# Performance work log

Measured on AMD Instinct MI355X. Metric: run time of the kernel, lower is better.

Reference implementation:

```python
import jax, jax.numpy as jnp
import numpy as np

D, N_EXP, TOP_K = 2048, 64, 8
B, S = 4, 4096

def setup_inputs() -> dict:
    key = jax.random.key(0)
    k1, k2, k3, k4 = jax.random.split(key, 4)
    hidden_states = jax.random.normal(k1, (B, S, D), dtype=jnp.float32)
    # nn.Linear weights are [out, in]; default init ~ U(-1/sqrt(d), 1/sqrt(d))
    bound = 1.0 / np.sqrt(D)
    W_gate = jax.random.uniform(k2, (N_EXP, D), jnp.float32, -bound, bound)
    W_noise = 0.01 * jax.random.normal(k3, (N_EXP, D), dtype=jnp.float32)
    # training-mode noise (router_step % top_k == 0 path): fixed-seed randn
    noise = jax.random.normal(k4, (B, S, N_EXP), dtype=jnp.float32)
    return {"hidden_states": hidden_states, "W_gate": W_gate,
            "W_noise": W_noise, "noise": noise}

def reference(hidden_states, W_gate, W_noise, noise):
    # logits = h @ W_gate^T  : [B,S,n_exp]
    logits = jnp.einsum('bsd,ed->bse', hidden_states, W_gate)
    scale = jax.nn.softplus(jnp.einsum('bsd,ed->bse', hidden_states, W_noise))
    logits = logits + noise * scale
    gates = jax.nn.softmax(logits, axis=-1)
    vals, inds = jax.lax.top_k(gates, TOP_K)  # sorted desc (torch used sorted=False)
    return vals, inds, gates
```

## Files before the change

kernel.cpp:

```cpp
#include <hip/hip_runtime.h>
#include <math.h>

typedef __attribute__((ext_vector_type(8))) _Float16 half8;
typedef __attribute__((ext_vector_type(4))) float    f32x4;

constexpr int D_DIM = 2048;
constexpr int NEXP  = 64;
constexpr int TOPK  = 8;
constexpr int NTOK  = 16384;
constexpr int TM    = 32;
constexpr int BK    = 64;
constexpr int NCH   = D_DIM / BK;
constexpr int OSTR  = 132;
constexpr int NSTR  = 68;
constexpr float WSCALE  = 4096.0f;
constexpr float INV_WSC = 1.0f / 4096.0f;

__device__ __forceinline__ unsigned short f16b(float x) {
    _Float16 h = (_Float16)x;
    return __builtin_bit_cast(unsigned short, h);
}
__device__ __forceinline__ float f16tof(unsigned short b) {
    return (float)__builtin_bit_cast(_Float16, b);
}

__global__ void prep_w(const float* __restrict__ Wg, const float* __restrict__ Wn,
                       unsigned short* __restrict__ wsB)
{
    const int idx = blockIdx.x * blockDim.x + threadIdx.x;
    const int n   = idx >> 8;
    const int K8  = idx & 255;
    const float* src = (n < 64) ? (Wg + (size_t)n * D_DIM)
                                : (Wn + (size_t)(n - 64) * D_DIM);
    float4 a = *reinterpret_cast<const float4*>(src + K8 * 8);
    float4 b = *reinterpret_cast<const float4*>(src + K8 * 8 + 4);

    float v[8] = {a.x, a.y, a.z, a.w, b.x, b.y, b.z, b.w};
    union { unsigned short u[8]; half8 s; } H, L;
#pragma unroll
    for (int j = 0; j < 8; ++j) {
        float xs = v[j] * WSCALE;
        unsigned short h = f16b(xs);
        H.u[j] = h;
        L.u[j] = f16b(xs - f16tof(h));
    }
    const int l = ((K8 & 3) * 16) + (n & 15);
    const size_t base = (size_t)(K8 >> 2) * 8192 + (size_t)(n >> 4) * 1024 + (size_t)l * 8;
    *reinterpret_cast<half8*>(wsB + base)       = H.s;
    *reinterpret_cast<half8*>(wsB + base + 512) = L.s;
}

__global__ __launch_bounds__(512, 4)
void noisy_topk_router(const float* __restrict__ hs,
                       const unsigned short* __restrict__ wsB,
                       const float* __restrict__ nz,
                       float* __restrict__ out)
{
    __shared__ __align__(16) char smem[16896 + 8704];
    unsigned short* stage  = reinterpret_cast<unsigned short*>(smem);
    float*          logits = reinterpret_cast<float*>(smem);
    float*          ldsN   = reinterpret_cast<float*>(smem + 16896);

    const int tid  = threadIdx.x;
    const int lane = tid & 63;
    const int w    = tid >> 6;
    const int t0   = blockIdx.x * TM;

    const int r  = tid >> 4;
    const int k4 = (tid & 15) * 4;
    const float* hrow = hs + (size_t)(t0 + r) * D_DIM + k4;
    const int ks_s = k4 >> 5;
    const int kk   = k4 & 31;
    const int j0   = kk >> 3;
    const int pos  = kk & 7;
    const int mt_s = r >> 4;
    const int m_s  = r & 15;
    const int wroff = (mt_s * 2 + ks_s) * 512 + (j0 * 16 + m_s) * 8 + pos;

    f32x4 accH0[2], accH1[2], accX[2];
#pragma unroll
    for (int mt = 0; mt < 2; ++mt) {
        accH0[mt] = (f32x4){0.f, 0.f, 0.f, 0.f};
        accH1[mt] = (f32x4){0.f, 0.f, 0.f, 0.f};
        accX[mt]  = (f32x4){0.f, 0.f, 0.f, 0.f};
    }

    auto cvt_write = [&](float4 v, unsigned short* buf) {
        float p[4] = {v.x, v.y, v.z, v.w};
        unsigned int Hp[2], Lp[2];
#pragma unroll
        for (int q = 0; q < 2; ++q) {
            unsigned short h0 = f16b(p[2*q]);
            unsigned short h1 = f16b(p[2*q+1]);
            unsigned short l0 = f16b(p[2*q]   - f16tof(h0));
            unsigned short l1 = f16b(p[2*q+1] - f16tof(h1));
            Hp[q] = (unsigned int)h0 | ((unsigned int)h1 << 16);
            Lp[q] = (unsigned int)l0 | ((unsigned int)l1 << 16);
        }
        *reinterpret_cast<uint2*>(buf + wroff)        = make_uint2(Hp[0], Hp[1]);
        *reinterpret_cast<uint2*>(buf + 2048 + wroff) = make_uint2(Lp[0], Lp[1]);
    };

    cvt_write(*reinterpret_cast<const float4*>(hrow), stage);
    __syncthreads();

    for (int c = 0; c < NCH; ++c) {
        float4 pf;
        if (c + 1 < NCH)
            pf = *reinterpret_cast<const float4*>(hrow + (c + 1) * BK);

        const unsigned short* sb = stage + (c & 1) * 4096;

#pragma unroll
        for (int ks = 0; ks < 2; ++ks) {
            const unsigned short* bp = wsB + (size_t)(2 * c + ks) * 8192
                                           + (size_t)w * 1024 + (size_t)lane * 8;
            half8 bhi = *reinterpret_cast<const half8*>(bp);
            half8 blo = *reinterpret_cast<const half8*>(bp + 512);
#pragma unroll
            for (int mt = 0; mt < 2; ++mt) {
                half8 ahi = *reinterpret_cast<const half8*>(sb + (mt * 2 + ks) * 512 + lane * 8);
                half8 alo = *reinterpret_cast<const half8*>(sb + 2048 + (mt * 2 + ks) * 512 + lane * 8);
                if (ks == 0)
                    accH0[mt] = __builtin_amdgcn_mfma_f32_16x16x32_f16(ahi, bhi, accH0[mt], 0, 0, 0);
                else
                    accH1[mt] = __builtin_amdgcn_mfma_f32_16x16x32_f16(ahi, bhi, accH1[mt], 0, 0, 0);
                accX[mt] = __builtin_amdgcn_mfma_f32_16x16x32_f16(ahi, blo, accX[mt], 0, 0, 0);
                accX[mt] = __builtin_amdgcn_mfma_f32_16x16x32_f16(alo, bhi, accX[mt], 0, 0, 0);
            }
        }

        if (c + 1 < NCH)
            cvt_write(pf, stage + ((c + 1) & 1) * 4096);
        __syncthreads();
    }

    {
        const int colb = w * 16 + (lane & 15);
        const int rowb = (lane >> 4) * 4;
#pragma unroll
        for (int mt = 0; mt < 2; ++mt)
#pragma unroll
            for (int rr = 0; rr < 4; ++rr)
                logits[(mt * 16 + rowb + rr) * OSTR + colb] =
                    (accH0[mt][rr] + accH1[mt][rr] + accX[mt][rr]) * INV_WSC;
    }
    {
        const int rr = tid >> 4;
        const int cc = tid & 15;
        float4 v = *reinterpret_cast<const float4*>(nz + (size_t)(t0 + rr) * NEXP + cc * 4);
        *reinterpret_cast<float4*>(&ldsN[rr * NSTR + cc * 4]) = v;
    }
    __syncthreads();

    if (tid < TM) {
        const int tok = t0 + tid;
        float l[NEXP];
        float mx = -3.0e38f;
#pragma unroll
        for (int e = 0; e < NEXP; ++e) {
            float gsc = logits[tid * OSTR + e];
            float nl  = logits[tid * OSTR + 64 + e];
            float sp  = fmaxf(nl, 0.0f) + log1pf(expf(-fabsf(nl)));
            float le  = fmaf(ldsN[tid * NSTR + e], sp, gsc);
            l[e] = le;
            mx = fmaxf(mx, le);
        }
        float sum = 0.0f;
#pragma unroll
        for (int e = 0; e < NEXP; ++e) { float p = expf(l[e] - mx); l[e] = p; sum += p; }
        float inv = 1.0f / sum;
#pragma unroll
        for (int e = 0; e < NEXP; ++e) l[e] *= inv;

#pragma unroll
        for (int e = 0; e < NEXP; ++e) logits[tid * OSTR + e] = l[e];

        float* vout = out + (size_t)tok * TOPK;
        float* iout = out + (size_t)NTOK * TOPK + (size_t)tok * TOPK;
#pragma unroll
        for (int p = 0; p < TOPK; ++p) {
            float m = -1.0f; int mi = 0;
#pragma unroll
            for (int e = 0; e < NEXP; ++e) {
                bool gt = l[e] > m;
                m  = gt ? l[e] : m;
                mi = gt ? e : mi;
            }
            vout[p] = m;
            iout[p] = (float)mi;
#pragma unroll
            for (int e = 0; e < NEXP; ++e) l[e] = (e == mi) ? -1.0f : l[e];
        }
    }
    __syncthreads();

    {
        const int rr = tid >> 4;
        const int cc = tid & 15;
        float* gout = out + (size_t)NTOK * TOPK * 2;
        float4 v = *reinterpret_cast<const float4*>(&logits[rr * OSTR + cc * 4]);
        *reinterpret_cast<float4*>(&gout[(size_t)(t0 + rr) * NEXP + cc * 4]) = v;
    }
}

extern "C" void kernel_launch(void* const* d_in, const int* in_sizes, int n_in,
                              void* d_out, int out_size, void* d_ws, size_t ws_size,
                              hipStream_t stream) {
    const float* hs = (const float*)d_in[0];
    const float* Wg = (const float*)d_in[1];
    const float* Wn = (const float*)d_in[2];
    const float* nz = (const float*)d_in[3];
    float* out = (float*)d_out;
    unsigned short* wsB = (unsigned short*)d_ws;

    prep_w<<<64, 512, 0, stream>>>(Wg, Wn, wsB);
    noisy_topk_router<<<NTOK / TM, 512, 0, stream>>>(hs, wsB, nz, out);
}
```

Baseline: 245.0 us.

## Retile router GEMM with register-prefetched weights and wave-parallel softmax/top-k epilogue

Doubles the K chunk to 128 and re-partitions waves so each wave covers one M tile and two N tiles, reusing each A fragment across two B tiles. Weight fragments are held in registers and prefetched two k-steps ahead, and the LDS staging layout gets an XOR swizzle to reduce bank conflicts. The epilogue now spreads softmax and top-k over all waves using lane-per-expert shuffle reductions, where before only 32 threads did serial per-token loops. The cost is more live registers and twice the LDS staging space, which could lower occupancy under the 512x4 launch bounds.

```diff
diff --git a/kernel.cpp b/kernel.cpp
--- a/kernel.cpp
+++ b/kernel.cpp
@@ -9,10 +9,10 @@
 constexpr int TOPK  = 8;
 constexpr int NTOK  = 16384;
 constexpr int TM    = 32;
-constexpr int BK    = 64;
+constexpr int BK    = 128;
 constexpr int NCH   = D_DIM / BK;
+constexpr int NKS   = D_DIM / 32;
 constexpr int OSTR  = 132;
-constexpr int NSTR  = 68;
 constexpr float WSCALE  = 4096.0f;
 constexpr float INV_WSC = 1.0f / 4096.0f;
 
@@ -56,151 +56,167 @@
                        const float* __restrict__ nz,
                        float* __restrict__ out)
 {
-    __shared__ __align__(16) char smem[16896 + 8704];
+    __shared__ __align__(16) char smem[32768];
     unsigned short* stage  = reinterpret_cast<unsigned short*>(smem);
     float*          logits = reinterpret_cast<float*>(smem);
-    float*          ldsN   = reinterpret_cast<float*>(smem + 16896);
 
     const int tid  = threadIdx.x;
     const int lane = tid & 63;
     const int w    = tid >> 6;
+    const int mt   = w & 1;
+    const int np   = w >> 1;
     const int t0   = blockIdx.x * TM;
 
-    const int r  = tid >> 4;
-    const int k4 = (tid & 15) * 4;
-    const float* hrow = hs + (size_t)(t0 + r) * D_DIM + k4;
-    const int ks_s = k4 >> 5;
-    const int kk   = k4 & 31;
-    const int j0   = kk >> 3;
-    const int pos  = kk & 7;
-    const int mt_s = r >> 4;
-    const int m_s  = r & 15;
-    const int wroff = (mt_s * 2 + ks_s) * 512 + (j0 * 16 + m_s) * 8 + pos;
-
-    f32x4 accH0[2], accH1[2], accX[2];
-#pragma unroll
-    for (int mt = 0; mt < 2; ++mt) {
-        accH0[mt] = (f32x4){0.f, 0.f, 0.f, 0.f};
-        accH1[mt] = (f32x4){0.f, 0.f, 0.f, 0.f};
-        accX[mt]  = (f32x4){0.f, 0.f, 0.f, 0.f};
-    }
-
-    auto cvt_write = [&](float4 v, unsigned short* buf) {
-        float p[4] = {v.x, v.y, v.z, v.w};
-        unsigned int Hp[2], Lp[2];
-#pragma unroll
-        for (int q = 0; q < 2; ++q) {
-            unsigned short h0 = f16b(p[2*q]);
-            unsigned short h1 = f16b(p[2*q+1]);
-            unsigned short l0 = f16b(p[2*q]   - f16tof(h0));
-            unsigned short l1 = f16b(p[2*q+1] - f16tof(h1));
-            Hp[q] = (unsigned int)h0 | ((unsigned int)h1 << 16);
-            Lp[q] = (unsigned int)l0 | ((unsigned int)l1 << 16);
-        }
-        *reinterpret_cast<uint2*>(buf + wroff)        = make_uint2(Hp[0], Hp[1]);
-        *reinterpret_cast<uint2*>(buf + 2048 + wroff) = make_uint2(Lp[0], Lp[1]);
+    const int j0r = lane >> 4;
+    const int mr  = lane & 15;
+    const int j4  = (j0r & 1) << 2;
+
+    const int r    = tid >> 4;
+    const int q    = tid & 15;
+    const int ks_s = q >> 2;
+    const int j0s  = q & 3;
+    const int ms   = r & 15;
+    const int mts  = r >> 4;
+    const int fs   = ks_s | ((j0s & 1) << 2);
+    const int wroff = (mts * 4 + ks_s) * 512 + (j0s * 16 + (ms ^ fs)) * 8;
+    const float* hrow = hs + (size_t)(t0 + r) * D_DIM + q * 8;
+
+    const unsigned short* bbase = wsB + (size_t)np * 2048 + (size_t)lane * 8;
+
+    f32x4 accP0[2], accP1[2], accX0[2], accX1[2];
+#pragma unroll
+    for (int nt = 0; nt < 2; ++nt) {
+        accP0[nt] = (f32x4){0.f, 0.f, 0.f, 0.f};
+        accP1[nt] = (f32x4){0.f, 0.f, 0.f, 0.f};
+        accX0[nt] = (f32x4){0.f, 0.f, 0.f, 0.f};
+        accX1[nt] = (f32x4){0.f, 0.f, 0.f, 0.f};
+    }
+
+    half8 bh[2][2], bl[2][2];
+#pragma unroll
+    for (int s = 0; s < 2; ++s)
+#pragma unroll
+        for (int nt = 0; nt < 2; ++nt) {
+            const unsigned short* bp = bbase + (size_t)s * 8192 + nt * 1024;
+            bh[s][nt] = *reinterpret_cast<const half8*>(bp);
+            bl[s][nt] = *reinterpret_cast<const half8*>(bp + 512);
+        }
+
+    auto cvt_write = [&](float4 a, float4 b, unsigned short* buf) {
+        float v[8] = {a.x, a.y, a.z, a.w, b.x, b.y, b.z, b.w};
+        union { unsigned short u[8]; half8 s; } H, L;
+#pragma unroll
+        for (int j = 0; j < 8; ++j) {
+            unsigned short h = f16b(v[j]);
+            H.u[j] = h;
+            L.u[j] = f16b(v[j] - f16tof(h));
+        }
+        *reinterpret_cast<half8*>(buf + wroff)        = H.s;
+        *reinterpret_cast<half8*>(buf + wroff + 4096) = L.s;
     };
 
-    cvt_write(*reinterpret_cast<const float4*>(hrow), stage);
+    {
+        float4 a = *reinterpret_cast<const float4*>(hrow);
+        float4 b = *reinterpret_cast<const float4*>(hrow + 4);
+        cvt_write(a, b, stage);
+    }
     __syncthreads();
 
     for (int c = 0; c < NCH; ++c) {
-        float4 pf;
+        float4 pa, pb;
+        if (c + 1 < NCH) {
+            pa = *reinterpret_cast<const float4*>(hrow + (c + 1) * BK);
+            pb = *reinterpret_cast<const float4*>(hrow + (c + 1) * BK + 4);
+        }
+        const unsigned short* sb = stage + (c & 1) * 8192;
+
+#pragma unroll
+        for (int ks = 0; ks < 4; ++ks) {
+            const int kk   = c * 4 + ks;
+            const int slot = ks & 1;
+            const int off  = (mt * 4 + ks) * 512
+                           + (j0r * 16 + (mr ^ (ks | j4))) * 8;
+            half8 ahi = *reinterpret_cast<const half8*>(sb + off);
+            half8 alo = *reinterpret_cast<const half8*>(sb + off + 4096);
+#pragma unroll
+            for (int nt = 0; nt < 2; ++nt) {
+                if ((ks & 1) == 0)
+                    accP0[nt] = __builtin_amdgcn_mfma_f32_16x16x32_f16(ahi, bh[slot][nt], accP0[nt], 0, 0, 0);
+                else
+                    accP1[nt] = __builtin_amdgcn_mfma_f32_16x16x32_f16(ahi, bh[slot][nt], accP1[nt], 0, 0, 0);
+                accX0[nt] = __builtin_amdgcn_mfma_f32_16x16x32_f16(ahi, bl[slot][nt], accX0[nt], 0, 0, 0);
+                accX1[nt] = __builtin_amdgcn_mfma_f32_16x16x32_f16(alo, bh[slot][nt], accX1[nt], 0, 0, 0);
+            }
+            if (ks < 2 || c + 1 < NCH) {
+                const unsigned short* bp2 = bbase + (size_t)(kk + 2) * 8192;
+#pragma unroll
+                for (int nt = 0; nt < 2; ++nt) {
+                    bh[slot][nt] = *reinterpret_cast<const half8*>(bp2 + nt * 1024);
+                    bl[slot][nt] = *reinterpret_cast<const half8*>(bp2 + nt * 1024 + 512);
+                }
+            }
+        }
+
         if (c + 1 < NCH)
-            pf = *reinterpret_cast<const float4*>(hrow + (c + 1) * BK);
-
-        const unsigned short* sb = stage + (c & 1) * 4096;
-
-#pragma unroll
-        for (int ks = 0; ks < 2; ++ks) {
-            const unsigned short* bp = wsB + (size_t)(2 * c + ks) * 8192
-                                           + (size_t)w * 1024 + (size_t)lane * 8;
-            half8 bhi = *reinterpret_cast<const half8*>(bp);
-            half8 blo = *reinterpret_cast<const half8*>(bp + 512);
-#pragma unroll
-            for (int mt = 0; mt < 2; ++mt) {
-                half8 ahi = *reinterpret_cast<const half8*>(sb + (mt * 2 + ks) * 512 + lane * 8);
-                half8 alo = *reinterpret_cast<const half8*>(sb + 2048 + (mt * 2 + ks) * 512 + lane * 8);
-                if (ks == 0)
-                    accH0[mt] = __builtin_amdgcn_mfma_f32_16x16x32_f16(ahi, bhi, accH0[mt], 0, 0, 0);
-                else
-                    accH1[mt] = __builtin_amdgcn_mfma_f32_16x16x32_f16(ahi, bhi, accH1[mt], 0, 0, 0);
-                accX[mt] = __builtin_amdgcn_mfma_f32_16x16x32_f16(ahi, blo, accX[mt], 0, 0, 0);
-                accX[mt] = __builtin_amdgcn_mfma_f32_16x16x32_f16(alo, bhi, accX[mt], 0, 0, 0);
+            cvt_write(pa, pb, stage + ((c + 1) & 1) * 8192);
+        __syncthreads();
+    }
+
+    {
+        const int colb = np * 32 + (lane & 15);
+        const int rowb = mt * 16 + (lane >> 4) * 4;
+#pragma unroll
+        for (int nt = 0; nt < 2; ++nt)
+#pragma unroll
+            for (int rr = 0; rr < 4; ++rr)
+                logits[(rowb + rr) * OSTR + colb + nt * 16] =
+                    (accP0[nt][rr] + accP1[nt][rr] + accX0[nt][rr] + accX1[nt][rr]) * INV_WSC;
+    }
+    __syncthreads();
+
+    float* gout = out + (size_t)NTOK * TOPK * 2;
+    for (int tt = 0; tt < 4; ++tt) {
+        const int tl  = w * 4 + tt;
+        const int tok = t0 + tl;
+        float gsc = logits[tl * OSTR + lane];
+        float nl  = logits[tl * OSTR + 64 + lane];
+        float nzv = nz[(size_t)tok * NEXP + lane];
+        float sp  = fmaxf(nl, 0.0f) + log1pf(expf(-fabsf(nl)));
+        float le  = fmaf(nzv, sp, gsc);
+
+        float mx = le;
+#pragma unroll
+        for (int d = 32; d > 0; d >>= 1) mx = fmaxf(mx, __shfl_xor(mx, d));
+        float pe = expf(le - mx);
+        float s  = pe;
+#pragma unroll
+        for (int d = 32; d > 0; d >>= 1) s += __shfl_xor(s, d);
+        float g = pe * (1.0f / s);
+
+        gout[(size_t)tok * NEXP + lane] = g;
+
+        float v = g;
+        float keepv = 0.0f;
+        int   keepi = 0;
+#pragma unroll
+        for (int it = 0; it < TOPK; ++it) {
+            float m  = v;
+            int   mi = lane;
+#pragma unroll
+            for (int d = 32; d > 0; d >>= 1) {
+                float om = __shfl_xor(m, d);
+                int   oi = __shfl_xor(mi, d);
+                bool take = (om > m) || (om == m && oi < mi);
+                m  = take ? om : m;
+                mi = take ? oi : mi;
             }
-        }
-
-        if (c + 1 < NCH)
-            cvt_write(pf, stage + ((c + 1) & 1) * 4096);
-        __syncthreads();
-    }
-
-    {
-        const int colb = w * 16 + (lane & 15);
-        const int rowb = (lane >> 4) * 4;
-#pragma unroll
-        for (int mt = 0; mt < 2; ++mt)
-#pragma unroll
-            for (int rr = 0; rr < 4; ++rr)
-                logits[(mt * 16 + rowb + rr) * OSTR + colb] =
-                    (accH0[mt][rr] + accH1[mt][rr] + accX[mt][rr]) * INV_WSC;
-    }
-    {
-        const int rr = tid >> 4;
-        const int cc = tid & 15;
-        float4 v = *reinterpret_cast<const float4*>(nz + (size_t)(t0 + rr) * NEXP + cc * 4);
-        *reinterpret_cast<float4*>(&ldsN[rr * NSTR + cc * 4]) = v;
-    }
-    __syncthreads();
-
-    if (tid < TM) {
-        const int tok = t0 + tid;
-        float l[NEXP];
-        float mx = -3.0e38f;
-#pragma unroll
-        for (int e = 0; e < NEXP; ++e) {
-            float gsc = logits[tid * OSTR + e];
-            float nl  = logits[tid * OSTR + 64 + e];
-            float sp  = fmaxf(nl, 0.0f) + log1pf(expf(-fabsf(nl)));
-            float le  = fmaf(ldsN[tid * NSTR + e], sp, gsc);
-            l[e] = le;
-            mx = fmaxf(mx, le);
-        }
-        float sum = 0.0f;
-#pragma unroll
-        for (int e = 0; e < NEXP; ++e) { float p = expf(l[e] - mx); l[e] = p; sum += p; }
-        float inv = 1.0f / sum;
-#pragma unroll
-        for (int e = 0; e < NEXP; ++e) l[e] *= inv;
-
-#pragma unroll
-        for (int e = 0; e < NEXP; ++e) logits[tid * OSTR + e] = l[e];
-
-        float* vout = out + (size_t)tok * TOPK;
-        float* iout = out + (size_t)NTOK * TOPK + (size_t)tok * TOPK;
-#pragma unroll
-        for (int p = 0; p < TOPK; ++p) {
-            float m = -1.0f; int mi = 0;
-#pragma unroll
-            for (int e = 0; e < NEXP; ++e) {
-                bool gt = l[e] > m;
-                m  = gt ? l[e] : m;
-                mi = gt ? e : mi;
-            }
-            vout[p] = m;
-            iout[p] = (float)mi;
-#pragma unroll
-            for (int e = 0; e < NEXP; ++e) l[e] = (e == mi) ? -1.0f : l[e];
-        }
-    }
-    __syncthreads();
-
-    {
-        const int rr = tid >> 4;
-        const int cc = tid & 15;
-        float* gout = out + (size_t)NTOK * TOPK * 2;
-        float4 v = *reinterpret_cast<const float4*>(&logits[rr * OSTR + cc * 4]);
-        *reinterpret_cast<float4*>(&gout[(size_t)(t0 + rr) * NEXP + cc * 4]) = v;
+            if (lane == it) { keepv = m; keepi = mi; }
+            if (lane == mi) v = -1.0f;
+        }
+        if (lane < TOPK) {
+            out[(size_t)tok * TOPK + lane] = keepv;
+            out[(size_t)NTOK * TOPK + (size_t)tok * TOPK + lane] = (float)keepi;
+        }
     }
 }
 
```

Result: faster. 233.4 us (-4.7%).
